# Kernel optimization log

Measured on AMD Instinct MI355X. Metric: run time of the kernel, lower is better.

## Reference

```python
import jax, jax.numpy as jnp
import numpy as np

DIM = 128          # observed dim
LATENT = 128       # SDE state_size
HID = 128          # mu hidden width (hard-coded in source)
BROWNIAN = 2       # brownian_size
N_STEPS = 200      # Euler-Maruyama steps over t in [0, 1]
DT = 1.0 / N_STEPS


def _linear_init(key, fan_in, fan_out):
    # torch nn.Linear default: U(-1/sqrt(fan_in), 1/sqrt(fan_in))
    kw, kb = jax.random.split(key)
    bound = 1.0 / np.sqrt(fan_in)
    w = jax.random.uniform(kw, (fan_in, fan_out), jnp.float32, -bound, bound)
    b = jax.random.uniform(kb, (fan_out,), jnp.float32, -bound, bound)
    return w, b


def setup_inputs() -> dict:
    key = jax.random.key(0)
    ks = jax.random.split(key, 8)
    y = jax.random.normal(ks[0], (32768, DIM), jnp.float32)
    noise = jax.random.normal(ks[1], (N_STEPS, 32768, BROWNIAN), jnp.float32)
    enc_w, enc_b = _linear_init(ks[2], DIM, LATENT)
    mu_w1, mu_b1 = _linear_init(ks[3], LATENT, HID)
    mu_w2, mu_b2 = _linear_init(ks[4], HID, LATENT)
    sig_w, sig_b = _linear_init(ks[5], LATENT, LATENT * BROWNIAN)
    dec_w, dec_b = _linear_init(ks[6], LATENT, DIM)
    return {
        "y": y, "noise": noise,
        "enc_w": enc_w, "enc_b": enc_b,
        "mu_w1": mu_w1, "mu_b1": mu_b1, "mu_w2": mu_w2, "mu_b2": mu_b2,
        "sig_w": sig_w, "sig_b": sig_b,
        "dec_w": dec_w, "dec_b": dec_b,
    }


def reference(y, noise, enc_w, enc_b, mu_w1, mu_b1, mu_w2, mu_b2, sig_w, sig_b, dec_w, dec_b):
    B = y.shape[0]
    # encoder: Linear + exact GELU (torch nn.GELU default)
    z0 = jax.nn.gelu(y @ enc_w + enc_b, approximate=False)

    sqrt_dt = jnp.asarray(np.sqrt(DT), jnp.float32)

    def drift(z):  # f(t, y) = mu(y)
        h = jax.nn.gelu(z @ mu_w1 + mu_b1, approximate=False)
        return h @ mu_w2 + mu_b2

    def diffusion(z):  # g(t, y) -> [B, state, brownian]
        return (z @ sig_w + sig_b).reshape(B, LATENT, BROWNIAN)

    def step(z, xi):
        # Euler-Maruyama (Ito): z += f*dt + g @ dW,  dW = sqrt(dt)*xi
        dW = xi * sqrt_dt                      # [B, K]
        g = diffusion(z)                       # [B, D, K]
        z = z + drift(z) * DT + jnp.einsum("bdk,bk->bd", g, dW)
        return z, None

    zT, _ = jax.lax.scan(step, z0, noise)
    return zT @ dec_w + dec_b
```

## Files before the change

### kernel.cpp

```cpp
#include <hip/hip_runtime.h>
#include <math.h>

#define NSTEPS 200
#define NT     512
#define BR     64
#define SQDT_F 0.07071067811865475f
#define DT_F   0.005f
#define LOSCL  4096.0f
#define LOINV  2.44140625e-4f

typedef float  f32x4 __attribute__((ext_vector_type(4)));
typedef short  s16x8 __attribute__((ext_vector_type(8)));
typedef _Float16 h16x8 __attribute__((ext_vector_type(8)));
typedef unsigned short u16;
typedef unsigned short us4 __attribute__((ext_vector_type(4)));

#define ENC_OFF 0
#define W1_OFF  32768
#define W2_OFF  65536
#define WG0_OFF 98304
#define WG1_OFF 131072
#define DEC_OFF 163840
#define WPK_TOT 196608

#define FO(kc, mt, term) (((((kc) * 4 + (mt)) * 2) + (term)) * 512)

__device__ __forceinline__ u16 f2h(float v) {
    _Float16 h = (_Float16)v;
    return __builtin_bit_cast(u16, h);
}
__device__ __forceinline__ float h2f(u16 u) {
    return (float)__builtin_bit_cast(_Float16, u);
}
__device__ __forceinline__ u16 split_hi(float v) { return f2h(v); }
__device__ __forceinline__ u16 split_lo(float v, u16 hi) {
    return f2h((v - h2f(hi)) * LOSCL);
}

__device__ __forceinline__ float gelu_fast(float x) {
    float ax = fabsf(x) * 0.70710678118654752f;
    float t  = __builtin_amdgcn_rcpf(fmaf(0.3275911f, ax, 1.0f));
    float p  = fmaf(t, 1.061405429f, -1.453152027f);
    p = fmaf(t, p, 1.421413741f);
    p = fmaf(t, p, -0.284496736f);
    p = fmaf(t, p, 0.254829592f);
    p = p * t;
    float e  = __expf(-ax * ax);
    float er = fmaf(-p, e, 1.0f);
    er = copysignf(er, x);
    return 0.5f * x * (1.0f + er);
}

__device__ __forceinline__ void mfma16(f32x4& d, s16x8 a, s16x8 b) {
    d = __builtin_amdgcn_mfma_f32_16x16x32_f16(
            __builtin_bit_cast(h16x8, a), __builtin_bit_cast(h16x8, b), d, 0, 0, 0);
}
__device__ __forceinline__ s16x8 ldf(const u16* p) {
    return *reinterpret_cast<const s16x8*>(p);
}

__global__ void prepack(const float* __restrict__ enc_w, const float* __restrict__ mu_w1,
                        const float* __restrict__ mu_w2, const float* __restrict__ sig_w,
                        const float* __restrict__ dec_w, u16* __restrict__ wpk)
{
    int u = blockIdx.x * 256 + threadIdx.x;
    if (u >= WPK_TOT) return;
    int mat  = u >> 15;
    int r    = u & 32767;
    int i    = r & 7;
    int lane = (r >> 3) & 63;
    int term = (r >> 9) & 1;
    int kc   = (r >> 10) & 3;
    int nt   = (r >> 12) & 7;
    int k = kc * 32 + 16 * (i >> 2) + 4 * (lane >> 4) + (i & 3);
    int n = nt * 16 + (lane & 15);
    float v;
    switch (mat) {
        case 0:  v = enc_w[k * 128 + n];         break;
        case 1:  v = mu_w1[k * 128 + n];         break;
        case 2:  v = mu_w2[k * 128 + n];         break;
        case 3:  v = sig_w[k * 256 + 2 * n];     break;
        case 4:  v = sig_w[k * 256 + 2 * n + 1]; break;
        default: v = dec_w[k * 128 + n];         break;
    }
    u16 hi = split_hi(v);
    wpk[u] = term ? split_lo(v, hi) : hi;
}

__global__ __launch_bounds__(NT) void sde_mfma(
    const float* __restrict__ y, const float* __restrict__ noise,
    const float* __restrict__ enc_b, const float* __restrict__ mu_b1,
    const float* __restrict__ mu_b2, const float* __restrict__ sig_b,
    const float* __restrict__ dec_b, const u16* __restrict__ wpk,
    float* __restrict__ out, int Btot)
{
    __shared__ __align__(16) u16 zx[16384];
    __shared__ __align__(16) u16 hx[16384];
    __shared__ float bb[4][128];
    __shared__ float nsb[2][128];

    const int tid  = threadIdx.x;
    const int lane = tid & 63, jt = tid >> 6;
    const int ln   = lane & 15, lg = lane >> 4;
    const size_t brow = (size_t)blockIdx.x * BR;

    const int jb  = 16 * jt + 4 * lg;
    const int pub = FO(jt >> 1, 0, 0) + lane * 8 + 4 * (jt & 1);

    if (tid < 128)      bb[0][tid]       = mu_b1[tid];
    else if (tid < 256) bb[1][tid - 128] = mu_b2[tid - 128];
    else if (tid < 384) bb[2][tid - 256] = sig_b[2 * (tid - 256)];
    else                bb[3][tid - 384] = sig_b[2 * (tid - 384) + 1];
    volatile const float* vb = &bb[0][0];

    #pragma unroll
    for (int cc = 0; cc < 4; cc++) {
        int q = cc * NT + tid;
        int m = q >> 5, cq = (q & 31) << 2;
        const float4 v = *reinterpret_cast<const float4*>(y + (brow + m) * 128 + cq);
        int kc = cq >> 5, a = (cq >> 4) & 1, b = (cq >> 2) & 3;
        int ad = FO(kc, m >> 4, 0) + ((m & 15) + 16 * b) * 8 + 4 * a;
        float vv[4] = {v.x, v.y, v.z, v.w};
        us4 hv, lv;
        #pragma unroll
        for (int e = 0; e < 4; e++) {
            u16 h = split_hi(vv[e]);
            hv[e] = h; lv[e] = split_lo(vv[e], h);
        }
        *reinterpret_cast<us4*>(zx + ad)       = hv;
        *reinterpret_cast<us4*>(zx + ad + 512) = lv;
    }
    __syncthreads();

    float zm[4][4];

    {
        f32x4 eb;
        #pragma unroll
        for (int r = 0; r < 4; r++) eb[r] = enc_b[jb + r];
        f32x4 a0[4], a1[4];
        #pragma unroll
        for (int mt = 0; mt < 4; mt++) { a0[mt] = eb; a1[mt] = f32x4{0, 0, 0, 0}; }
        #pragma unroll 2
        for (int kc = 0; kc < 4; kc++) {
            const u16* ap = wpk + ENC_OFF + ((jt * 4 + kc) * 2) * 512 + lane * 8;
            s16x8 wh = ldf(ap), wl = ldf(ap + 512);
            #pragma unroll
            for (int mt = 0; mt < 4; mt++) {
                int zo = FO(kc, mt, 0) + lane * 8;
                s16x8 zh_ = ldf(zx + zo), zl_ = ldf(zx + zo + 512);
                mfma16(a0[mt], wh, zh_);
                mfma16(a1[mt], wl, zh_);
                mfma16(a1[mt], wh, zl_);
            }
        }
        #pragma unroll
        for (int mt = 0; mt < 4; mt++)
            #pragma unroll
            for (int r = 0; r < 4; r++)
                zm[mt][r] = gelu_fast(fmaf(a1[mt][r], LOINV, a0[mt][r]));
    }
    __syncthreads();

    #pragma unroll
    for (int mt = 0; mt < 4; mt++) {
        us4 hv, lv;
        #pragma unroll
        for (int r = 0; r < 4; r++) {
            u16 h = split_hi(zm[mt][r]);
            hv[r] = h; lv[r] = split_lo(zm[mt][r], h);
        }
        int ad = pub + mt * 1024;
        *reinterpret_cast<us4*>(zx + ad)       = hv;
        *reinterpret_cast<us4*>(zx + ad + 512) = lv;
    }
    if (tid < 128) nsb[0][tid] = noise[brow * 2 + tid];
    __syncthreads();

    const u16* wq = wpk;

    for (int t = 0; t < NSTEPS; t++) {
        asm volatile("" : "+s"(wq));
        {
            int tn = (t + 1 < NSTEPS) ? (t + 1) : t;
            if (tid < 128) nsb[(t + 1) & 1][tid] = noise[((size_t)tn * Btot + brow) * 2 + tid];
        }
        {
            f32x4 b1v;
            #pragma unroll
            for (int r = 0; r < 4; r++) b1v[r] = vb[0 * 128 + jb + r];
            f32x4 a0[4], a1[4];
            #pragma unroll
            for (int mt = 0; mt < 4; mt++) { a0[mt] = b1v; a1[mt] = f32x4{0, 0, 0, 0}; }
            #pragma unroll 2
            for (int kc = 0; kc < 4; kc++) {
                const u16* ap = wq + W1_OFF + ((jt * 4 + kc) * 2) * 512 + lane * 8;
                s16x8 wh = ldf(ap), wl = ldf(ap + 512);
                #pragma unroll
                for (int mt = 0; mt < 4; mt++) {
                    int zo = FO(kc, mt, 0) + lane * 8;
                    s16x8 zh_ = ldf(zx + zo), zl_ = ldf(zx + zo + 512);
                    mfma16(a0[mt], wh, zh_);
                    mfma16(a1[mt], wl, zh_);
                    mfma16(a1[mt], wh, zl_);
                }
            }
            #pragma unroll
            for (int mt = 0; mt < 4; mt++) {
                us4 hv, lv;
                #pragma unroll
                for (int r = 0; r < 4; r++) {
                    float h = gelu_fast(fmaf(a1[mt][r], LOINV, a0[mt][r]));
                    u16 hh = split_hi(h);
                    hv[r] = hh; lv[r] = split_lo(h, hh);
                }
                int ad = pub + mt * 1024;
                *reinterpret_cast<us4*>(hx + ad)       = hv;
                *reinterpret_cast<us4*>(hx + ad + 512) = lv;
            }
        }
        {
            f32x4 g0v, g1v;
            #pragma unroll
            for (int r = 0; r < 4; r++) {
                g0v[r] = vb[2 * 128 + jb + r];
                g1v[r] = vb[3 * 128 + jb + r];
            }
            f32x4 q0h[4], q0l[4], q1h[4], q1l[4];
            #pragma unroll
            for (int mt = 0; mt < 4; mt++) {
                q0h[mt] = g0v; q0l[mt] = f32x4{0, 0, 0, 0};
                q1h[mt] = g1v; q1l[mt] = f32x4{0, 0, 0, 0};
            }
            #pragma unroll 2
            for (int kc = 0; kc < 4; kc++) {
                const u16* p0 = wq + WG0_OFF + ((jt * 4 + kc) * 2) * 512 + lane * 8;
                const u16* p1 = wq + WG1_OFF + ((jt * 4 + kc) * 2) * 512 + lane * 8;
                s16x8 w0h = ldf(p0), w0l = ldf(p0 + 512);
                s16x8 w1h = ldf(p1), w1l = ldf(p1 + 512);
                #pragma unroll
                for (int mt = 0; mt < 4; mt++) {
                    int zo = FO(kc, mt, 0) + lane * 8;
                    s16x8 zh_ = ldf(zx + zo), zl_ = ldf(zx + zo + 512);
                    mfma16(q0h[mt], w0h, zh_);
                    mfma16(q0l[mt], w0l, zh_);
                    mfma16(q0l[mt], w0h, zl_);
                    mfma16(q1h[mt], w1h, zh_);
                    mfma16(q1l[mt], w1l, zh_);
                    mfma16(q1l[mt], w1h, zl_);
                }
            }
            const float* np = nsb[t & 1];
            #pragma unroll
            for (int mt = 0; mt < 4; mt++) {
                int mrow = ln + 16 * mt;
                float dw0 = np[2 * mrow] * SQDT_F;
                float dw1 = np[2 * mrow + 1] * SQDT_F;
                #pragma unroll
                for (int r = 0; r < 4; r++) {
                    float gv0 = fmaf(q0l[mt][r], LOINV, q0h[mt][r]);
                    float gv1 = fmaf(q1l[mt][r], LOINV, q1h[mt][r]);
                    zm[mt][r] = fmaf(gv0, dw0, fmaf(gv1, dw1, zm[mt][r]));
                }
            }
        }
        __syncthreads();

        {
            f32x4 b2v;
            #pragma unroll
            for (int r = 0; r < 4; r++) b2v[r] = vb[1 * 128 + jb + r];
            f32x4 a0[4], a1[4];
            #pragma unroll
            for (int mt = 0; mt < 4; mt++) { a0[mt] = b2v; a1[mt] = f32x4{0, 0, 0, 0}; }
            #pragma unroll 2
            for (int kc = 0; kc < 4; kc++) {
                const u16* ap = wq + W2_OFF + ((jt * 4 + kc) * 2) * 512 + lane * 8;
                s16x8 wh = ldf(ap), wl = ldf(ap + 512);
                #pragma unroll
                for (int mt = 0; mt < 4; mt++) {
                    int ho = FO(kc, mt, 0) + lane * 8;
                    s16x8 hh_ = ldf(hx + ho), hl_ = ldf(hx + ho + 512);
                    mfma16(a0[mt], wh, hh_);
                    mfma16(a1[mt], wl, hh_);
                    mfma16(a1[mt], wh, hl_);
                }
            }
            #pragma unroll
            for (int mt = 0; mt < 4; mt++) {
                us4 hv, lv;
                #pragma unroll
                for (int r = 0; r < 4; r++) {
                    float drift = fmaf(a1[mt][r], LOINV, a0[mt][r]);
                    float v = fmaf(drift, DT_F, zm[mt][r]);
                    zm[mt][r] = v;
                    u16 hh = split_hi(v);
                    hv[r] = hh; lv[r] = split_lo(v, hh);
                }
                int ad = pub + mt * 1024;
                *reinterpret_cast<us4*>(zx + ad)       = hv;
                *reinterpret_cast<us4*>(zx + ad + 512) = lv;
            }
        }
        __syncthreads();
    }

    {
        f32x4 dbv;
        #pragma unroll
        for (int r = 0; r < 4; r++) dbv[r] = dec_b[jb + r];
        f32x4 a0[4], a1[4];
        #pragma unroll
        for (int mt = 0; mt < 4; mt++) { a0[mt] = dbv; a1[mt] = f32x4{0, 0, 0, 0}; }
        #pragma unroll 2
        for (int kc = 0; kc < 4; kc++) {
            const u16* ap = wpk + DEC_OFF + ((jt * 4 + kc) * 2) * 512 + lane * 8;
            s16x8 wh = ldf(ap), wl = ldf(ap + 512);
            #pragma unroll
            for (int mt = 0; mt < 4; mt++) {
                int zo = FO(kc, mt, 0) + lane * 8;
                s16x8 zh_ = ldf(zx + zo), zl_ = ldf(zx + zo + 512);
                mfma16(a0[mt], wh, zh_);
                mfma16(a1[mt], wl, zh_);
                mfma16(a1[mt], wh, zl_);
            }
        }
        #pragma unroll
        for (int mt = 0; mt < 4; mt++) {
            f32x4 o;
            #pragma unroll
            for (int r = 0; r < 4; r++) o[r] = fmaf(a1[mt][r], LOINV, a0[mt][r]);
            *reinterpret_cast<f32x4*>(out + (brow + ln + 16 * mt) * 128 + jb) = o;
        }
    }
}

extern "C" void kernel_launch(void* const* d_in, const int* in_sizes, int n_in,
                              void* d_out, int out_size, void* d_ws, size_t ws_size,
                              hipStream_t stream) {
    const float* y     = (const float*)d_in[0];
    const float* noise = (const float*)d_in[1];
    const float* enc_w = (const float*)d_in[2];
    const float* enc_b = (const float*)d_in[3];
    const float* mu_w1 = (const float*)d_in[4];
    const float* mu_b1 = (const float*)d_in[5];
    const float* mu_w2 = (const float*)d_in[6];
    const float* mu_b2 = (const float*)d_in[7];
    const float* sig_w = (const float*)d_in[8];
    const float* sig_b = (const float*)d_in[9];
    const float* dec_w = (const float*)d_in[10];
    const float* dec_b = (const float*)d_in[11];
    float* out = (float*)d_out;
    u16* wpk = (u16*)d_ws;

    const int Btot = in_sizes[0] / 128;
    prepack<<<(WPK_TOT + 255) / 256, 256, 0, stream>>>(enc_w, mu_w1, mu_w2, sig_w, dec_w, wpk);
    sde_mfma<<<Btot / BR, NT, 0, stream>>>(y, noise, enc_b, mu_b1, mu_b2, sig_b, dec_b,
                                           wpk, out, Btot);
}
```

Before: 2.738 ms.

## Fuse mu layer-1 and diffusion GEMMs sharing z fragments, split rows in halves

Merges the first drift layer and the two diffusion projections into one k-loop, so each z fragment loaded from LDS feeds nine MFMAs instead of being reloaded for two separate passes. To hold register pressure down, the 64-row tile is processed in two halves of 32 rows, with the k-loop no longer unrolled. Weight fragments are now loaded twice per step, once per half, trading extra weight loads and less unrolling for fewer z reloads and a lower peak accumulator count.

```diff
diff --git a/kernel.cpp b/kernel.cpp
--- a/kernel.cpp
+++ b/kernel.cpp
@@ -185,83 +185,68 @@
             int tn = (t + 1 < NSTEPS) ? (t + 1) : t;
             if (tid < 128) nsb[(t + 1) & 1][tid] = noise[((size_t)tn * Btot + brow) * 2 + tid];
         }
-        {
-            f32x4 b1v;
-            #pragma unroll
-            for (int r = 0; r < 4; r++) b1v[r] = vb[0 * 128 + jb + r];
-            f32x4 a0[4], a1[4];
-            #pragma unroll
-            for (int mt = 0; mt < 4; mt++) { a0[mt] = b1v; a1[mt] = f32x4{0, 0, 0, 0}; }
-            #pragma unroll 2
+        const float* np = nsb[t & 1];
+        #pragma unroll 1
+        for (int mh = 0; mh < 2; mh++) {
+            f32x4 b1v, g0v, g1v;
+            #pragma unroll
+            for (int r = 0; r < 4; r++) {
+                b1v[r] = vb[0 * 128 + jb + r];
+                g0v[r] = vb[2 * 128 + jb + r];
+                g1v[r] = vb[3 * 128 + jb + r];
+            }
+            f32x4 a0[2], a1[2], q0h[2], q0l[2], q1h[2], q1l[2];
+            #pragma unroll
+            for (int u = 0; u < 2; u++) {
+                a0[u]  = b1v; a1[u]  = f32x4{0, 0, 0, 0};
+                q0h[u] = g0v; q0l[u] = f32x4{0, 0, 0, 0};
+                q1h[u] = g1v; q1l[u] = f32x4{0, 0, 0, 0};
+            }
+            #pragma unroll 1
             for (int kc = 0; kc < 4; kc++) {
-                const u16* ap = wq + W1_OFF + ((jt * 4 + kc) * 2) * 512 + lane * 8;
-                s16x8 wh = ldf(ap), wl = ldf(ap + 512);
-                #pragma unroll
-                for (int mt = 0; mt < 4; mt++) {
-                    int zo = FO(kc, mt, 0) + lane * 8;
+                const u16* a1p = wq + W1_OFF  + ((jt * 4 + kc) * 2) * 512 + lane * 8;
+                const u16* p0  = wq + WG0_OFF + ((jt * 4 + kc) * 2) * 512 + lane * 8;
+                const u16* p1  = wq + WG1_OFF + ((jt * 4 + kc) * 2) * 512 + lane * 8;
+                s16x8 w1h_ = ldf(a1p), w1l_ = ldf(a1p + 512);
+                s16x8 w0h  = ldf(p0),  w0l  = ldf(p0 + 512);
+                s16x8 wg1h = ldf(p1),  wg1l = ldf(p1 + 512);
+                #pragma unroll
+                for (int u = 0; u < 2; u++) {
+                    int zo = FO(kc, 2 * mh + u, 0) + lane * 8;
                     s16x8 zh_ = ldf(zx + zo), zl_ = ldf(zx + zo + 512);
-                    mfma16(a0[mt], wh, zh_);
-                    mfma16(a1[mt], wl, zh_);
-                    mfma16(a1[mt], wh, zl_);
-                }
-            }
-            #pragma unroll
-            for (int mt = 0; mt < 4; mt++) {
+                    mfma16(a0[u],  w1h_, zh_);
+                    mfma16(a1[u],  w1l_, zh_);
+                    mfma16(a1[u],  w1h_, zl_);
+                    mfma16(q0h[u], w0h,  zh_);
+                    mfma16(q0l[u], w0l,  zh_);
+                    mfma16(q0l[u], w0h,  zl_);
+                    mfma16(q1h[u], wg1h, zh_);
+                    mfma16(q1l[u], wg1l, zh_);
+                    mfma16(q1l[u], wg1h, zl_);
+                }
+            }
+            #pragma unroll
+            for (int u = 0; u < 2; u++) {
+                const int mt = 2 * mh + u;
+                int mrow = ln + 16 * mt;
+                float dw0 = np[2 * mrow] * SQDT_F;
+                float dw1 = np[2 * mrow + 1] * SQDT_F;
+                #pragma unroll
+                for (int r = 0; r < 4; r++) {
+                    float gv0 = fmaf(q0l[u][r], LOINV, q0h[u][r]);
+                    float gv1 = fmaf(q1l[u][r], LOINV, q1h[u][r]);
+                    zm[mt][r] = fmaf(gv0, dw0, fmaf(gv1, dw1, zm[mt][r]));
+                }
                 us4 hv, lv;
                 #pragma unroll
                 for (int r = 0; r < 4; r++) {
-                    float h = gelu_fast(fmaf(a1[mt][r], LOINV, a0[mt][r]));
+                    float h = gelu_fast(fmaf(a1[u][r], LOINV, a0[u][r]));
                     u16 hh = split_hi(h);
                     hv[r] = hh; lv[r] = split_lo(h, hh);
                 }
                 int ad = pub + mt * 1024;
                 *reinterpret_cast<us4*>(hx + ad)       = hv;
                 *reinterpret_cast<us4*>(hx + ad + 512) = lv;
-            }
-        }
-        {
-            f32x4 g0v, g1v;
-            #pragma unroll
-            for (int r = 0; r < 4; r++) {
-                g0v[r] = vb[2 * 128 + jb + r];
-                g1v[r] = vb[3 * 128 + jb + r];
-            }
-            f32x4 q0h[4], q0l[4], q1h[4], q1l[4];
-            #pragma unroll
-            for (int mt = 0; mt < 4; mt++) {
-                q0h[mt] = g0v; q0l[mt] = f32x4{0, 0, 0, 0};
-                q1h[mt] = g1v; q1l[mt] = f32x4{0, 0, 0, 0};
-            }
-            #pragma unroll 2
-            for (int kc = 0; kc < 4; kc++) {
-                const u16* p0 = wq + WG0_OFF + ((jt * 4 + kc) * 2) * 512 + lane * 8;
-                const u16* p1 = wq + WG1_OFF + ((jt * 4 + kc) * 2) * 512 + lane * 8;
-                s16x8 w0h = ldf(p0), w0l = ldf(p0 + 512);
-                s16x8 w1h = ldf(p1), w1l = ldf(p1 + 512);
-                #pragma unroll
-                for (int mt = 0; mt < 4; mt++) {
-                    int zo = FO(kc, mt, 0) + lane * 8;
-                    s16x8 zh_ = ldf(zx + zo), zl_ = ldf(zx + zo + 512);
-                    mfma16(q0h[mt], w0h, zh_);
-                    mfma16(q0l[mt], w0l, zh_);
-                    mfma16(q0l[mt], w0h, zl_);
-                    mfma16(q1h[mt], w1h, zh_);
-                    mfma16(q1l[mt], w1l, zh_);
-                    mfma16(q1l[mt], w1h, zl_);
-                }
-            }
-            const float* np = nsb[t & 1];
-            #pragma unroll
-            for (int mt = 0; mt < 4; mt++) {
-                int mrow = ln + 16 * mt;
-                float dw0 = np[2 * mrow] * SQDT_F;
-                float dw1 = np[2 * mrow + 1] * SQDT_F;
-                #pragma unroll
-                for (int r = 0; r < 4; r++) {
-                    float gv0 = fmaf(q0l[mt][r], LOINV, q0h[mt][r]);
-                    float gv1 = fmaf(q1l[mt][r], LOINV, q1h[mt][r]);
-                    zm[mt][r] = fmaf(gv0, dw0, fmaf(gv1, dw1, zm[mt][r]));
-                }
             }
         }
         __syncthreads();
```

New measurement: 3.130 ms. +14.3%, slower.
